# Performance work log

Measured on AMD Instinct MI355X. Metric: run time of the kernel, lower is better.

The kernel has to match this reference:

```python
import jax, jax.numpy as jnp
import numpy as np

N, C, F = 8192, 128, 128
ALPHA = 0.2
BETA = 0.3
NEG = -9e15


def setup_inputs() -> dict:
    key = jax.random.key(0)
    k1, k2, k3, k4 = jax.random.split(key, 4)
    h = jax.random.normal(k1, (N, C), dtype=jnp.float32)
    adj = jax.random.randint(k2, (N, N), 0, 2, dtype=jnp.int32)
    w = jax.random.normal(k3, (C, F), dtype=jnp.float32) * 0.1
    a = jax.random.normal(k4, (N, 2 * F, 1), dtype=jnp.float32) * 0.1
    return {"h": h, "adj": adj, "batch_i": 0, "w": w, "a": a}


def reference(h, adj, batch_i, w, a):
    # Wh: [N, F]
    Wh = h @ w
    # Per-row attention vectors: a[i] = [a1[i]; a2[i]], each [F].
    # Original builds a_input[i,j] = [Wh[i], Wh[j]] (O(N^2*2F)) then dots with a[i].
    # Equivalent: e[i,j] = Wh[i].a1[i] + Wh[j].a2[i]  -- computed without the huge tensor.
    a1 = a[:, :F, 0]  # [N, F]
    a2 = a[:, F:, 0]  # [N, F]
    s1 = jnp.sum(Wh * a1, axis=1)           # [N]
    e = s1[:, None] + a2 @ Wh.T             # [N, N]
    e = jnp.where(e > 0, e, ALPHA * e)      # LeakyReLU
    e = jnp.where(adj > 0, e, NEG)          # mask non-edges
    attention = jax.nn.softmax(e, axis=1)   # [N, N]
    h_prime = attention @ Wh                # [N, F]
    out = jax.nn.elu(h_prime + BETA * Wh)
    return out
```

## Files before the change

kernel.cpp:

```cpp
#include <hip/hip_runtime.h>
#include <hip/hip_bf16.h>
#include <stdint.h>
#include <math.h>

#define N_NODES 8192
#define FDIM 128
#define LRELU_ALPHA 0.2f
#define BETA 0.3f
#define NEGV -9000000000000000.0f
#define THR 8.0f

typedef __attribute__((ext_vector_type(8))) short bf16x8;
typedef __attribute__((ext_vector_type(4))) float f32x4;

__device__ __forceinline__ uint16_t f2b(float x) {
  union { float f; uint32_t u; } v; v.f = x;
  uint32_t r = v.u + 0x7FFFu + ((v.u >> 16) & 1u);
  return (uint16_t)(r >> 16);
}

__global__ void __launch_bounds__(256) prep_wh(
    const float* __restrict__ h, const float* __restrict__ w,
    float* __restrict__ whf, uint16_t* __restrict__ whb,
    uint16_t* __restrict__ whtb) {
  __shared__ float hs[32][128];
  const int t = threadIdx.x;
  const int rb = blockIdx.x * 32;
#pragma unroll
  for (int k = 0; k < 16; ++k) {
    int idx = t + k * 256;
    int r = idx >> 7, c = idx & 127;
    hs[r][c] = h[(size_t)(rb + r) * FDIM + c];
  }
  __syncthreads();
  const int c = t & 127;
  const int half = t >> 7;
  const int r0 = half * 16;
  float acc[16];
#pragma unroll
  for (int k = 0; k < 16; ++k) acc[k] = 0.f;
  for (int kk = 0; kk < 128; ++kk) {
    float wv = w[kk * FDIM + c];
#pragma unroll
    for (int k = 0; k < 16; ++k) acc[k] += hs[r0 + k][kk] * wv;
  }
  uint16_t tb[16];
#pragma unroll
  for (int k = 0; k < 16; ++k) {
    int r = rb + r0 + k;
    whf[(size_t)r * FDIM + c] = acc[k];
    uint16_t b = f2b(acc[k]);
    whb[(size_t)r * FDIM + c] = b;
    tb[k] = b;
  }
  uint16_t* dst = whtb + (size_t)c * N_NODES + rb + r0;
  bf16x8 v0, v1;
#pragma unroll
  for (int k = 0; k < 8; ++k) { v0[k] = (short)tb[k]; v1[k] = (short)tb[k + 8]; }
  *(bf16x8*)(dst) = v0;
  *(bf16x8*)(dst + 8) = v1;
}

__global__ void __launch_bounds__(256) prep_s1(
    const float* __restrict__ whf, const float* __restrict__ a,
    float* __restrict__ s1, uint16_t* __restrict__ a2b) {
  const int t = threadIdx.x;
  const int rb = blockIdx.x * 32;
  const int wv = t >> 6;
  const int lane = t & 63;
  const int r = rb + wv * 8 + (lane >> 3);
  const int c0 = (lane & 7) * 16;
  float s = 0.f;
#pragma unroll
  for (int k = 0; k < 16; ++k) {
    s += whf[(size_t)r * FDIM + c0 + k] * a[(size_t)r * 256 + c0 + k];
  }
  s += __shfl_xor(s, 1);
  s += __shfl_xor(s, 2);
  s += __shfl_xor(s, 4);
  if ((lane & 7) == 0) s1[r] = s;
#pragma unroll
  for (int k = 0; k < 16; ++k) {
    int idx = t + k * 256;
    int rr = idx >> 7, cc = idx & 127;
    a2b[(size_t)(rb + rr) * FDIM + cc] = f2b(a[(size_t)(rb + rr) * 256 + 128 + cc]);
  }
}

__global__ void __launch_bounds__(512, 2) gat_main(
    const int* __restrict__ adj, const uint16_t* __restrict__ whb,
    const uint16_t* __restrict__ whtb, const uint16_t* __restrict__ a2b,
    const float* __restrict__ s1, const float* __restrict__ whf,
    float* __restrict__ out) {
  __shared__ float O_lds[8][16][128];
  __shared__ __align__(16) uint16_t plds[8][32][40];
  __shared__ float m_lds[8][32], l_lds[8][32];
  __shared__ float ew_lds[8][32], linv_lds[32];

  const int tid = threadIdx.x;
  const int wv = tid >> 6;
  const int lane = tid & 63;
  const int ln = lane & 15;
  const int lg = lane >> 4;
  const int ibase = blockIdx.x * 32;

  bf16x8 af[2][4];
#pragma unroll
  for (int it = 0; it < 2; ++it)
#pragma unroll
    for (int ks = 0; ks < 4; ++ks)
      af[it][ks] = *(const bf16x8*)(a2b + (size_t)(ibase + it * 16 + ln) * FDIM + ks * 32 + lg * 8);

  float s1v[2][4];
#pragma unroll
  for (int it = 0; it < 2; ++it)
#pragma unroll
    for (int r = 0; r < 4; ++r)
      s1v[it][r] = s1[ibase + it * 16 + lg * 4 + r];

  const int* adjbase = adj + (size_t)(ibase + lg * 4) * N_NODES + ln;

  float mrun[2][4], lsum[2][4];
#pragma unroll
  for (int it = 0; it < 2; ++it)
#pragma unroll
    for (int r = 0; r < 4; ++r) { mrun[it][r] = -INFINITY; lsum[it][r] = 0.f; }
  f32x4 O[2][8];
#pragma unroll
  for (int it = 0; it < 2; ++it)
#pragma unroll
    for (int ft = 0; ft < 8; ++ft) O[it][ft] = (f32x4){0.f, 0.f, 0.f, 0.f};

  const int j0 = wv * (N_NODES / 8);
  for (int jb = j0; jb < j0 + N_NODES / 8; jb += 32) {
    int adjv[2][2][4];
#pragma unroll
    for (int it = 0; it < 2; ++it)
#pragma unroll
      for (int nt = 0; nt < 2; ++nt)
#pragma unroll
        for (int r = 0; r < 4; ++r)
          adjv[it][nt][r] = adjbase[(size_t)(it * 16 + r) * N_NODES + jb + nt * 16];

    f32x4 sacc[2][2];
#pragma unroll
    for (int it = 0; it < 2; ++it)
#pragma unroll
      for (int nt = 0; nt < 2; ++nt) sacc[it][nt] = (f32x4){0.f, 0.f, 0.f, 0.f};
#pragma unroll
    for (int nt = 0; nt < 2; ++nt)
#pragma unroll
      for (int ks = 0; ks < 4; ++ks) {
        bf16x8 b = *(const bf16x8*)(whb + (size_t)(jb + nt * 16 + ln) * FDIM + ks * 32 + lg * 8);
        sacc[0][nt] = __builtin_amdgcn_mfma_f32_16x16x32_bf16(af[0][ks], b, sacc[0][nt], 0, 0, 0);
        sacc[1][nt] = __builtin_amdgcn_mfma_f32_16x16x32_bf16(af[1][ks], b, sacc[1][nt], 0, 0, 0);
      }

    float e[2][2][4];
#pragma unroll
    for (int it = 0; it < 2; ++it)
#pragma unroll
      for (int nt = 0; nt < 2; ++nt)
#pragma unroll
        for (int r = 0; r < 4; ++r) {
          float v = s1v[it][r] + sacc[it][nt][r];
          v = (v > 0.f) ? v : LRELU_ALPHA * v;
          e[it][nt][r] = (adjv[it][nt][r] > 0) ? v : NEGV;
        }

    bool upd = false;
#pragma unroll
    for (int it = 0; it < 2; ++it)
#pragma unroll
      for (int r = 0; r < 4; ++r)
        upd |= (e[it][0][r] > mrun[it][r] + THR) || (e[it][1][r] > mrun[it][r] + THR);
    if (__any(upd)) {
#pragma unroll
      for (int it = 0; it < 2; ++it) {
        float mx[4];
#pragma unroll
        for (int r = 0; r < 4; ++r) mx[r] = fmaxf(e[it][0][r], e[it][1][r]);
#pragma unroll
        for (int off = 1; off <= 8; off <<= 1)
#pragma unroll
          for (int r = 0; r < 4; ++r) mx[r] = fmaxf(mx[r], __shfl_xor(mx[r], off));
#pragma unroll
        for (int r = 0; r < 4; ++r) {
          float mn = fmaxf(mrun[it][r], mx[r]);
          float al = __expf(mrun[it][r] - mn);
          mrun[it][r] = mn;
          lsum[it][r] *= al;
#pragma unroll
          for (int ft = 0; ft < 8; ++ft) O[it][ft][r] *= al;
        }
      }
    }

#pragma unroll
    for (int it = 0; it < 2; ++it)
#pragma unroll
      for (int nt = 0; nt < 2; ++nt)
#pragma unroll
        for (int r = 0; r < 4; ++r) {
          float p = __expf(e[it][nt][r] - mrun[it][r]);
          lsum[it][r] += p;
          plds[wv][it * 16 + lg * 4 + r][nt * 16 + ln] = f2b(p);
        }

    bf16x8 pa0 = *(const bf16x8*)&plds[wv][ln][lg * 8];
    bf16x8 pa1 = *(const bf16x8*)&plds[wv][16 + ln][lg * 8];

#pragma unroll
    for (int ft = 0; ft < 8; ++ft) {
      bf16x8 bv = *(const bf16x8*)(whtb + (size_t)(ft * 16 + ln) * N_NODES + jb + lg * 8);
      O[0][ft] = __builtin_amdgcn_mfma_f32_16x16x32_bf16(pa0, bv, O[0][ft], 0, 0, 0);
      O[1][ft] = __builtin_amdgcn_mfma_f32_16x16x32_bf16(pa1, bv, O[1][ft], 0, 0, 0);
    }
  }

#pragma unroll
  for (int off = 1; off <= 8; off <<= 1)
#pragma unroll
    for (int it = 0; it < 2; ++it)
#pragma unroll
      for (int r = 0; r < 4; ++r) lsum[it][r] += __shfl_xor(lsum[it][r], off);

  if (ln == 0) {
#pragma unroll
    for (int it = 0; it < 2; ++it)
#pragma unroll
      for (int r = 0; r < 4; ++r) {
        m_lds[wv][it * 16 + lg * 4 + r] = mrun[it][r];
        l_lds[wv][it * 16 + lg * 4 + r] = lsum[it][r];
      }
  }
  __syncthreads();

  if (tid < 32) {
    float ms = -INFINITY;
#pragma unroll
    for (int w2 = 0; w2 < 8; ++w2) ms = fmaxf(ms, m_lds[w2][tid]);
    float L = 0.f;
#pragma unroll
    for (int w2 = 0; w2 < 8; ++w2) {
      float x = __expf(m_lds[w2][tid] - ms);
      ew_lds[w2][tid] = x;
      L += l_lds[w2][tid] * x;
    }
    linv_lds[tid] = 1.0f / L;
  }
  __syncthreads();

#pragma unroll
  for (int h = 0; h < 2; ++h) {
#pragma unroll
    for (int ft = 0; ft < 8; ++ft)
#pragma unroll
      for (int r = 0; r < 4; ++r)
        O_lds[wv][lg * 4 + r][ft * 16 + ln] = O[h][ft][r];
    __syncthreads();
#pragma unroll
    for (int k = 0; k < 4; ++k) {
      int idx = tid + k * 512;
      int r = idx >> 7, f = idx & 127;
      float v = 0.f;
#pragma unroll
      for (int w2 = 0; w2 < 8; ++w2) v += O_lds[w2][r][f] * ew_lds[w2][h * 16 + r];
      v *= linv_lds[h * 16 + r];
      int row = ibase + h * 16 + r;
      v += BETA * whf[(size_t)row * FDIM + f];
      out[(size_t)row * FDIM + f] = (v > 0.f) ? v : (__expf(v) - 1.0f);
    }
    if (h == 0) __syncthreads();
  }
}

extern "C" void kernel_launch(void* const* d_in, const int* in_sizes, int n_in,
                              void* d_out, int out_size, void* d_ws, size_t ws_size,
                              hipStream_t stream) {
  const float* h   = (const float*)d_in[0];
  const int*   adj = (const int*)d_in[1];
  const float* w   = (const float*)d_in[3];
  const float* a   = (const float*)d_in[4];
  float* out = (float*)d_out;

  char* ws = (char*)d_ws;
  float*    whf  = (float*)ws;
  uint16_t* whb  = (uint16_t*)(ws + (4 << 20));
  uint16_t* whtb = (uint16_t*)(ws + (6 << 20));
  uint16_t* a2b  = (uint16_t*)(ws + (8 << 20));
  float*    s1   = (float*)(ws + (10 << 20));

  prep_wh<<<N_NODES / 32, 256, 0, stream>>>(h, w, whf, whb, whtb);
  prep_s1<<<N_NODES / 32, 256, 0, stream>>>(whf, a, s1, a2b);
  gat_main<<<N_NODES / 32, 512, 0, stream>>>(adj, whb, whtb, a2b, s1, whf, out);
}
```

Measured before the change: 168.6 us.

## Transpose score MFMA so rows map to lanes, pass P via shuffles

Swaps the MFMA operands for the score tile so each lane owns one query row and four contiguous columns. This allows the adjacency mask to be loaded as 16-byte vectors and cuts the row max/sum reductions to two cross-group shuffles. The P tile is handed to the second MFMA through register shuffles with truncating bf16 packing instead of an LDS round trip. In exchange the rescale factors must be broadcast by shuffle, and truncation replaces round-to-nearest for P.

After: 190.6 us. +13.1%, slower.

```diff
diff --git a/kernel.cpp b/kernel.cpp
--- a/kernel.cpp
+++ b/kernel.cpp
@@ -12,6 +12,7 @@
 
 typedef __attribute__((ext_vector_type(8))) short bf16x8;
 typedef __attribute__((ext_vector_type(4))) float f32x4;
+typedef __attribute__((ext_vector_type(4))) int i32x4;
 
 __device__ __forceinline__ uint16_t f2b(float x) {
   union { float f; uint32_t u; } v; v.f = x;
@@ -93,7 +94,6 @@
     const float* __restrict__ s1, const float* __restrict__ whf,
     float* __restrict__ out) {
   __shared__ float O_lds[8][16][128];
-  __shared__ __align__(16) uint16_t plds[8][32][40];
   __shared__ float m_lds[8][32], l_lds[8][32];
   __shared__ float ew_lds[8][32], linv_lds[32];
 
@@ -111,20 +111,15 @@
     for (int ks = 0; ks < 4; ++ks)
       af[it][ks] = *(const bf16x8*)(a2b + (size_t)(ibase + it * 16 + ln) * FDIM + ks * 32 + lg * 8);
 
-  float s1v[2][4];
-#pragma unroll
-  for (int it = 0; it < 2; ++it)
-#pragma unroll
-    for (int r = 0; r < 4; ++r)
-      s1v[it][r] = s1[ibase + it * 16 + lg * 4 + r];
-
-  const int* adjbase = adj + (size_t)(ibase + lg * 4) * N_NODES + ln;
-
-  float mrun[2][4], lsum[2][4];
-#pragma unroll
-  for (int it = 0; it < 2; ++it)
-#pragma unroll
-    for (int r = 0; r < 4; ++r) { mrun[it][r] = -INFINITY; lsum[it][r] = 0.f; }
+  float s1v[2];
+#pragma unroll
+  for (int it = 0; it < 2; ++it) s1v[it] = s1[ibase + it * 16 + ln];
+
+  const size_t adjr0 = (size_t)(ibase + ln) * N_NODES;
+  const size_t adjr1 = (size_t)(ibase + 16 + ln) * N_NODES;
+
+  float mrun[2] = {-INFINITY, -INFINITY};
+  float lsum[2] = {0.f, 0.f};
   f32x4 O[2][8];
 #pragma unroll
   for (int it = 0; it < 2; ++it)
@@ -133,14 +128,11 @@
 
   const int j0 = wv * (N_NODES / 8);
   for (int jb = j0; jb < j0 + N_NODES / 8; jb += 32) {
-    int adjv[2][2][4];
-#pragma unroll
-    for (int it = 0; it < 2; ++it)
-#pragma unroll
-      for (int nt = 0; nt < 2; ++nt)
-#pragma unroll
-        for (int r = 0; r < 4; ++r)
-          adjv[it][nt][r] = adjbase[(size_t)(it * 16 + r) * N_NODES + jb + nt * 16];
+    i32x4 adjv[2][2];
+    adjv[0][0] = *(const i32x4*)(adj + adjr0 + jb + lg * 4);
+    adjv[0][1] = *(const i32x4*)(adj + adjr0 + jb + 16 + lg * 4);
+    adjv[1][0] = *(const i32x4*)(adj + adjr1 + jb + lg * 4);
+    adjv[1][1] = *(const i32x4*)(adj + adjr1 + jb + 16 + lg * 4);
 
     f32x4 sacc[2][2];
 #pragma unroll
@@ -152,8 +144,8 @@
 #pragma unroll
       for (int ks = 0; ks < 4; ++ks) {
         bf16x8 b = *(const bf16x8*)(whb + (size_t)(jb + nt * 16 + ln) * FDIM + ks * 32 + lg * 8);
-        sacc[0][nt] = __builtin_amdgcn_mfma_f32_16x16x32_bf16(af[0][ks], b, sacc[0][nt], 0, 0, 0);
-        sacc[1][nt] = __builtin_amdgcn_mfma_f32_16x16x32_bf16(af[1][ks], b, sacc[1][nt], 0, 0, 0);
+        sacc[0][nt] = __builtin_amdgcn_mfma_f32_16x16x32_bf16(b, af[0][ks], sacc[0][nt], 0, 0, 0);
+        sacc[1][nt] = __builtin_amdgcn_mfma_f32_16x16x32_bf16(b, af[1][ks], sacc[1][nt], 0, 0, 0);
       }
 
     float e[2][2][4];
@@ -163,7 +155,7 @@
       for (int nt = 0; nt < 2; ++nt)
 #pragma unroll
         for (int r = 0; r < 4; ++r) {
-          float v = s1v[it][r] + sacc[it][nt][r];
+          float v = s1v[it] + sacc[it][nt][r];
           v = (v > 0.f) ? v : LRELU_ALPHA * v;
           e[it][nt][r] = (adjv[it][nt][r] > 0) ? v : NEGV;
         }
@@ -172,67 +164,96 @@
 #pragma unroll
     for (int it = 0; it < 2; ++it)
 #pragma unroll
-      for (int r = 0; r < 4; ++r)
-        upd |= (e[it][0][r] > mrun[it][r] + THR) || (e[it][1][r] > mrun[it][r] + THR);
+      for (int nt = 0; nt < 2; ++nt)
+#pragma unroll
+        for (int r = 0; r < 4; ++r) upd |= (e[it][nt][r] > mrun[it] + THR);
     if (__any(upd)) {
 #pragma unroll
       for (int it = 0; it < 2; ++it) {
-        float mx[4];
-#pragma unroll
-        for (int r = 0; r < 4; ++r) mx[r] = fmaxf(e[it][0][r], e[it][1][r]);
-#pragma unroll
-        for (int off = 1; off <= 8; off <<= 1)
-#pragma unroll
-          for (int r = 0; r < 4; ++r) mx[r] = fmaxf(mx[r], __shfl_xor(mx[r], off));
-#pragma unroll
-        for (int r = 0; r < 4; ++r) {
-          float mn = fmaxf(mrun[it][r], mx[r]);
-          float al = __expf(mrun[it][r] - mn);
-          mrun[it][r] = mn;
-          lsum[it][r] *= al;
-#pragma unroll
-          for (int ft = 0; ft < 8; ++ft) O[it][ft][r] *= al;
+        float mx = e[it][0][0];
+#pragma unroll
+        for (int nt = 0; nt < 2; ++nt)
+#pragma unroll
+          for (int r = 0; r < 4; ++r) mx = fmaxf(mx, e[it][nt][r]);
+        mx = fmaxf(mx, __shfl_xor(mx, 16));
+        mx = fmaxf(mx, __shfl_xor(mx, 32));
+        float mn = fmaxf(mrun[it], mx);
+        float al = __expf(mrun[it] - mn);
+        mrun[it] = mn;
+        lsum[it] *= al;
+        float alb0 = __shfl(al, lg * 4 + 0);
+        float alb1 = __shfl(al, lg * 4 + 1);
+        float alb2 = __shfl(al, lg * 4 + 2);
+        float alb3 = __shfl(al, lg * 4 + 3);
+#pragma unroll
+        for (int ft = 0; ft < 8; ++ft) {
+          O[it][ft][0] *= alb0;
+          O[it][ft][1] *= alb1;
+          O[it][ft][2] *= alb2;
+          O[it][ft][3] *= alb3;
         }
       }
     }
 
+    uint32_t W[2][2][2];
 #pragma unroll
     for (int it = 0; it < 2; ++it)
 #pragma unroll
-      for (int nt = 0; nt < 2; ++nt)
-#pragma unroll
-        for (int r = 0; r < 4; ++r) {
-          float p = __expf(e[it][nt][r] - mrun[it][r]);
-          lsum[it][r] += p;
-          plds[wv][it * 16 + lg * 4 + r][nt * 16 + ln] = f2b(p);
-        }
-
-    bf16x8 pa0 = *(const bf16x8*)&plds[wv][ln][lg * 8];
-    bf16x8 pa1 = *(const bf16x8*)&plds[wv][16 + ln][lg * 8];
+      for (int nt = 0; nt < 2; ++nt) {
+        union { float f; uint32_t u; } p0, p1, p2, p3;
+        p0.f = __expf(e[it][nt][0] - mrun[it]);
+        p1.f = __expf(e[it][nt][1] - mrun[it]);
+        p2.f = __expf(e[it][nt][2] - mrun[it]);
+        p3.f = __expf(e[it][nt][3] - mrun[it]);
+        lsum[it] += (p0.f + p1.f) + (p2.f + p3.f);
+        W[it][nt][0] = (p1.u & 0xFFFF0000u) | (p0.u >> 16);
+        W[it][nt][1] = (p3.u & 0xFFFF0000u) | (p2.u >> 16);
+      }
+
+    const int s01 = ln + ((lg & 1) << 5);
+    const int s23 = s01 + 16;
+    const bool hi = (lg >= 2);
+    union PW { uint32_t w[4]; bf16x8 v; } pw0, pw1;
+    {
+      uint32_t a0 = __shfl((int)W[0][0][0], s01), b0 = __shfl((int)W[0][1][0], s01);
+      uint32_t a1 = __shfl((int)W[0][0][1], s01), b1 = __shfl((int)W[0][1][1], s01);
+      uint32_t a2 = __shfl((int)W[0][0][0], s23), b2 = __shfl((int)W[0][1][0], s23);
+      uint32_t a3 = __shfl((int)W[0][0][1], s23), b3 = __shfl((int)W[0][1][1], s23);
+      pw0.w[0] = hi ? b0 : a0;
+      pw0.w[1] = hi ? b1 : a1;
+      pw0.w[2] = hi ? b2 : a2;
+      pw0.w[3] = hi ? b3 : a3;
+    }
+    {
+      uint32_t a0 = __shfl((int)W[1][0][0], s01), b0 = __shfl((int)W[1][1][0], s01);
+      uint32_t a1 = __shfl((int)W[1][0][1], s01), b1 = __shfl((int)W[1][1][1], s01);
+      uint32_t a2 = __shfl((int)W[1][0][0], s23), b2 = __shfl((int)W[1][1][0], s23);
+      uint32_t a3 = __shfl((int)W[1][0][1], s23), b3 = __shfl((int)W[1][1][1], s23);
+      pw1.w[0] = hi ? b0 : a0;
+      pw1.w[1] = hi ? b1 : a1;
+      pw1.w[2] = hi ? b2 : a2;
+      pw1.w[3] = hi ? b3 : a3;
+    }
 
 #pragma unroll
     for (int ft = 0; ft < 8; ++ft) {
       bf16x8 bv = *(const bf16x8*)(whtb + (size_t)(ft * 16 + ln) * N_NODES + jb + lg * 8);
-      O[0][ft] = __builtin_amdgcn_mfma_f32_16x16x32_bf16(pa0, bv, O[0][ft], 0, 0, 0);
-      O[1][ft] = __builtin_amdgcn_mfma_f32_16x16x32_bf16(pa1, bv, O[1][ft], 0, 0, 0);
-    }
-  }
-
-#pragma unroll
-  for (int off = 1; off <= 8; off <<= 1)
-#pragma unroll
-    for (int it = 0; it < 2; ++it)
-#pragma unroll
-      for (int r = 0; r < 4; ++r) lsum[it][r] += __shfl_xor(lsum[it][r], off);
-
-  if (ln == 0) {
-#pragma unroll
-    for (int it = 0; it < 2; ++it)
-#pragma unroll
-      for (int r = 0; r < 4; ++r) {
-        m_lds[wv][it * 16 + lg * 4 + r] = mrun[it][r];
-        l_lds[wv][it * 16 + lg * 4 + r] = lsum[it][r];
-      }
+      O[0][ft] = __builtin_amdgcn_mfma_f32_16x16x32_bf16(pw0.v, bv, O[0][ft], 0, 0, 0);
+      O[1][ft] = __builtin_amdgcn_mfma_f32_16x16x32_bf16(pw1.v, bv, O[1][ft], 0, 0, 0);
+    }
+  }
+
+#pragma unroll
+  for (int it = 0; it < 2; ++it) {
+    lsum[it] += __shfl_xor(lsum[it], 16);
+    lsum[it] += __shfl_xor(lsum[it], 32);
+  }
+
+  if (lane < 16) {
+    m_lds[wv][lane] = mrun[0];
+    m_lds[wv][16 + lane] = mrun[1];
+    l_lds[wv][lane] = lsum[0];
+    l_lds[wv][16 + lane] = lsum[1];
   }
   __syncthreads();
 
```
